# Kernel optimization log

Measured on AMD Instinct MI355X. Metric: run time of the kernel, lower is better.

The kernel has to match this reference:

```python
import jax, jax.numpy as jnp
import numpy as np

BN_EPS = 1e-5


def setup_inputs() -> dict:
    key = jax.random.key(0)
    ks = jax.random.split(key, 16)
    N, E, IN, H, A, L = 50000, 400000, 128, 192, 192, 3
    s = 0.02
    inp = {
        "x": jax.random.normal(ks[0], (N, IN), dtype=jnp.float32),
        "edge_index": jax.random.randint(ks[1], (2, E), 0, N, dtype=jnp.int32),
        "seed_idx": 123,
        "proj_w": jax.random.normal(ks[2], (IN, H), dtype=jnp.float32) * s,
        "proj_b": jnp.zeros((H,), dtype=jnp.float32),
        "mlp1_w": jax.random.normal(ks[3], (L, H, H), dtype=jnp.float32) * s,
        "mlp1_b": jnp.zeros((L, H), dtype=jnp.float32),
        "mlp2_w": jax.random.normal(ks[4], (L, H, H), dtype=jnp.float32) * s,
        "mlp2_b": jnp.zeros((L, H), dtype=jnp.float32),
        "eps": jnp.zeros((L,), dtype=jnp.float32),  # GIN train_eps init 0
        "bn_g": jnp.ones((L, H), dtype=jnp.float32),
        "bn_b": jnp.zeros((L, H), dtype=jnp.float32),
        "W1": jax.random.normal(ks[5], (H, A), dtype=jnp.float32) * s,
        "W2": jax.random.normal(ks[6], (H, A), dtype=jnp.float32) * s,
        "w_attn": jax.random.normal(ks[7], (A,), dtype=jnp.float32) * s,
        "cls_w": jax.random.normal(ks[8], (H,), dtype=jnp.float32) * s,
        "cls_b": jnp.zeros((1,), dtype=jnp.float32),
    }
    return inp


def _forward(x, edge_index, seed_idx, proj_w, proj_b, mlp1_w, mlp1_b,
             mlp2_w, mlp2_b, eps, bn_g, bn_b, W1, W2, w_attn, cls_w, cls_b):
    N = x.shape[0]
    src, dst = edge_index[0], edge_index[1]
    h = jax.nn.relu(x @ proj_w + proj_b)  # [N, H]
    L = mlp1_w.shape[0]
    for l in range(L):
        # GINConv: mlp((1+eps)*h + sum_{j->i} h_j) via scatter-add on dst
        agg = jax.ops.segment_sum(h[src], dst, num_segments=N)  # [N, H]
        z = (1.0 + eps[l]) * h + agg
        z = jax.nn.relu(z @ mlp1_w[l] + mlp1_b[l]) @ mlp2_w[l] + mlp2_b[l]
        # BatchNorm over nodes (batch statistics)
        mu = z.mean(axis=0)
        var = z.var(axis=0)
        z = (z - mu) * jax.lax.rsqrt(var + BN_EPS) * bn_g[l] + bn_b[l]
        h = jax.nn.relu(z)  # dropout is identity in eval
    h_seed = h[seed_idx]  # valid seed index branch
    zat = jnp.tanh(h @ W1 + h_seed @ W2)          # [N, A]
    e = jax.nn.leaky_relu(zat @ w_attn, 0.2)      # [N]
    alpha = jax.nn.softmax(e, axis=0)             # [N]
    readout = alpha @ h                           # [H]
    logit = readout @ cls_w + cls_b               # [1]
    return logit, alpha


def reference(x, edge_index, seed_idx, proj_w, proj_b, mlp1_w, mlp1_b,
              mlp2_w, mlp2_b, eps, bn_g, bn_b, W1, W2, w_attn, cls_w, cls_b):
    return _forward(x, edge_index, seed_idx, proj_w, proj_b, mlp1_w, mlp1_b,
                    mlp2_w, mlp2_b, eps, bn_g, bn_b, W1, W2, w_attn, cls_w, cls_b)
```

## Files before the change

kernel.cpp:

```cpp
#include <hip/hip_runtime.h>
#include <hip/hip_bf16.h>

#define N_NODES 50000
#define N_EDGES 400000
#define DIM_IN  128
#define DIM_H   192
#define N_LAYERS 3
#define BN_EPSF 1e-5f
#define SCAN_NBLK 49
#define INV_N (1.f / N_NODES)
#define NSHADOW 8
#define SSTRIDE 384
#define WTP_BLOCKS 138

typedef __attribute__((ext_vector_type(8))) short short8;
typedef __attribute__((ext_vector_type(4))) float floatx4;

union FragU { uint4 u; short8 s; };

__device__ __forceinline__ float relu_f(float x) { return x > 0.f ? x : 0.f; }
__device__ __forceinline__ unsigned short f2bf(float x) {
  __hip_bfloat16 h = __float2bfloat16(x);
  return *reinterpret_cast<unsigned short*>(&h);
}
__device__ __forceinline__ float bf2f(unsigned short b) {
  return __uint_as_float(((unsigned)b) << 16);
}
__device__ __forceinline__ float bflo(unsigned u) { return __uint_as_float(u << 16); }
__device__ __forceinline__ float bfhi(unsigned u) { return __uint_as_float(u & 0xffff0000u); }

__device__ __forceinline__ unsigned char f2f8(float v) {
  return (unsigned char)(__builtin_amdgcn_cvt_pk_fp8_f32(v, v, 0, false) & 0xff);
}
template <int SEL>
__device__ __forceinline__ float f8dec(unsigned u) {
  return __builtin_amdgcn_cvt_f32_fp8((int)u, SEL);
}

__global__ void k_wtp_hist(const float* __restrict__ m1, const float* __restrict__ m2,
                           const float* __restrict__ wa, const float* __restrict__ pw,
                           uint4* __restrict__ outp,
                           const int* __restrict__ edge, int* __restrict__ cnt) {
  if (blockIdx.x < WTP_BLOCKS) {
    const int NH = 7 * 24 * 192;
    const int NP = 16 * 192;
    int idx = blockIdx.x * 256 + threadIdx.x;
    if (idx >= NH + NP) return;
    union { uint4 u; unsigned short h[8]; } fr;
    if (idx < NH) {
      int mat = idx / (24 * 192);
      int rem = idx - mat * (24 * 192);
      int kidx = rem / 192, col = rem - kidx * 192;
      const float* src = mat < 3 ? m1 + (size_t)mat * (DIM_H * DIM_H)
                       : (mat < 6 ? m2 + (size_t)(mat - 3) * (DIM_H * DIM_H) : wa);
#pragma unroll
      for (int t = 0; t < 8; ++t) fr.h[t] = f2bf(src[(size_t)(kidx * 8 + t) * DIM_H + col]);
    } else {
      int rem = idx - NH;
      int kidx = rem / 192, col = rem - kidx * 192;
#pragma unroll
      for (int t = 0; t < 8; ++t) fr.h[t] = f2bf(pw[(size_t)(kidx * 8 + t) * DIM_H + col]);
    }
    outp[idx] = fr.u;
  } else {
    int e = (blockIdx.x - WTP_BLOCKS) * 256 + threadIdx.x;
    if (e < N_EDGES) atomicAdd(&cnt[edge[N_EDGES + e]], 1);
  }
}

__global__ void k_scanA(const int* __restrict__ deg, int* __restrict__ part, int* __restrict__ bsum) {
  __shared__ int buf[1024];
  int g = blockIdx.x * 1024 + threadIdx.x;
  int v = (g < N_NODES) ? deg[g] : 0;
  buf[threadIdx.x] = v;
  __syncthreads();
  for (int off = 1; off < 1024; off <<= 1) {
    int t = (threadIdx.x >= off) ? buf[threadIdx.x - off] : 0;
    __syncthreads();
    buf[threadIdx.x] += t;
    __syncthreads();
  }
  if (g < N_NODES) part[g] = buf[threadIdx.x];
  if (threadIdx.x == 1023) bsum[blockIdx.x] = buf[1023];
}

__global__ void k_scanC(const int* __restrict__ part, const int* __restrict__ bsum,
                        int* __restrict__ rowptr, int* __restrict__ cursor) {
  __shared__ int excl[64];
  int tid = threadIdx.x;
  if (tid < 64) {
    int own = (tid < SCAN_NBLK) ? bsum[tid] : 0;
    int v = own;
    for (int off = 1; off < 64; off <<= 1) {
      int t = __shfl_up(v, off);
      if (tid >= off) v += t;
    }
    excl[tid] = v - own;
  }
  __syncthreads();
  int g = blockIdx.x * 256 + tid;
  if (g == 0) { rowptr[0] = 0; cursor[0] = 0; }
  if (g < N_NODES) {
    int v = part[g] + excl[g >> 10];
    rowptr[g + 1] = v;
    if (g + 1 < N_NODES) cursor[g + 1] = v;
  }
}

__global__ void k_fill(const int* __restrict__ edge, int* __restrict__ cursor, int* __restrict__ csr) {
  int e = blockIdx.x * 256 + threadIdx.x;
  if (e < N_EDGES) {
    int s = edge[e];
    int d = edge[N_EDGES + e];
    int pos = atomicAdd(&cursor[d], 1);
    csr[pos] = s;
  }
}

template <bool BN>
__global__ void k_agg(const unsigned char* __restrict__ z, const int* __restrict__ rowptr,
                      const int* __restrict__ csr, const float* __restrict__ stats,
                      const float* __restrict__ bng, const float* __restrict__ bnb,
                      const float* __restrict__ eps, int l, unsigned short* __restrict__ outA) {
  int wid = threadIdx.x >> 6, lane = threadIdx.x & 63;
  int node = blockIdx.x * 4 + wid;
  if (node >= N_NODES || lane >= 48) return;
  int c = lane * 4;
  float4 sc4 = {1.f, 1.f, 1.f, 1.f}, sh4 = {0.f, 0.f, 0.f, 0.f};
  if (BN) {
    float4 st = {0.f, 0.f, 0.f, 0.f}, sq = {0.f, 0.f, 0.f, 0.f};
#pragma unroll
    for (int g = 0; g < NSHADOW; ++g) {
      const float* sp = stats + g * SSTRIDE;
      float4 a = *(const float4*)(sp + c);
      float4 b = *(const float4*)(sp + DIM_H + c);
      st.x += a.x; st.y += a.y; st.z += a.z; st.w += a.w;
      sq.x += b.x; sq.y += b.y; sq.z += b.z; sq.w += b.w;
    }
    float4 g4 = *(const float4*)(bng + c);
    float4 b4 = *(const float4*)(bnb + c);
    float mu, rs;
    mu = st.x * INV_N; rs = rsqrtf(sq.x * INV_N - mu * mu + BN_EPSF); sc4.x = g4.x * rs; sh4.x = b4.x - mu * sc4.x;
    mu = st.y * INV_N; rs = rsqrtf(sq.y * INV_N - mu * mu + BN_EPSF); sc4.y = g4.y * rs; sh4.y = b4.y - mu * sc4.y;
    mu = st.z * INV_N; rs = rsqrtf(sq.z * INV_N - mu * mu + BN_EPSF); sc4.z = g4.z * rs; sh4.z = b4.z - mu * sc4.z;
    mu = st.w * INV_N; rs = rsqrtf(sq.w * INV_N - mu * mu + BN_EPSF); sc4.w = g4.w * rs; sh4.w = b4.w - mu * sc4.w;
  }
  float a0 = 0.f, a1 = 0.f, a2 = 0.f, a3 = 0.f;
  int beg = rowptr[node], end = rowptr[node + 1];
  unsigned us = *(const unsigned*)(z + (size_t)node * DIM_H + c);
#define ACCU(U)                                                          \
  {                                                                      \
    float v0 = f8dec<0>(U), v1 = f8dec<1>(U);                            \
    float v2 = f8dec<2>(U), v3 = f8dec<3>(U);                            \
    if (BN) {                                                            \
      v0 = relu_f(fmaf(v0, sc4.x, sh4.x));                               \
      v1 = relu_f(fmaf(v1, sc4.y, sh4.y));                               \
      v2 = relu_f(fmaf(v2, sc4.z, sh4.z));                               \
      v3 = relu_f(fmaf(v3, sc4.w, sh4.w));                               \
    }                                                                    \
    a0 += v0; a1 += v1; a2 += v2; a3 += v3;                              \
  }
  int j = beg;
  for (; j + 4 <= end; j += 4) {
    int s0 = csr[j], s1 = csr[j + 1], s2 = csr[j + 2], s3 = csr[j + 3];
    unsigned u0 = *(const unsigned*)(z + (size_t)s0 * DIM_H + c);
    unsigned u1 = *(const unsigned*)(z + (size_t)s1 * DIM_H + c);
    unsigned u2 = *(const unsigned*)(z + (size_t)s2 * DIM_H + c);
    unsigned u3 = *(const unsigned*)(z + (size_t)s3 * DIM_H + c);
    ACCU(u0) ACCU(u1) ACCU(u2) ACCU(u3)
  }
  for (; j < end; ++j) {
    int s0 = csr[j];
    unsigned u0 = *(const unsigned*)(z + (size_t)s0 * DIM_H + c);
    ACCU(u0)
  }
#undef ACCU
  float ep = 1.f + eps[l];
  {
    float v0 = f8dec<0>(us), v1 = f8dec<1>(us), v2 = f8dec<2>(us), v3 = f8dec<3>(us);
    if (BN) {
      v0 = relu_f(fmaf(v0, sc4.x, sh4.x));
      v1 = relu_f(fmaf(v1, sc4.y, sh4.y));
      v2 = relu_f(fmaf(v2, sc4.z, sh4.z));
      v3 = relu_f(fmaf(v3, sc4.w, sh4.w));
    }
    a0 += ep * v0; a1 += ep * v1; a2 += ep * v2; a3 += ep * v3;
  }
  uint2 o;
  o.x = (unsigned)f2bf(a0) | ((unsigned)f2bf(a1) << 16);
  o.y = (unsigned)f2bf(a2) | ((unsigned)f2bf(a3) << 16);
  *(uint2*)(outA + (size_t)node * DIM_H + c) = o;
}

template <int KS>
__device__ __forceinline__ void load_b(const uint4* __restrict__ Bp, int colbase, int kq, int lr,
                                       FragU (&b)[KS][3]) {
#pragma unroll
  for (int ks = 0; ks < KS; ++ks)
#pragma unroll
    for (int n = 0; n < 3; ++n)
      b[ks][n].u = Bp[(ks * 4 + kq) * 192 + colbase + n * 16 + lr];
}

template <int KS, int MT>
__device__ __forceinline__ void mfma_stage_pre(const uint4* a_lds, const FragU (&b)[KS][3],
                                               int kq, int lr, floatx4 (&acc)[MT][3]) {
#pragma unroll
  for (int ks = 0; ks < KS; ++ks) {
    int kidx = ks * 4 + kq;
    FragU a[MT];
#pragma unroll
    for (int m = 0; m < MT; ++m) a[m].u = a_lds[kidx * (MT * 16) + m * 16 + lr];
#pragma unroll
    for (int n = 0; n < 3; ++n)
#pragma unroll
      for (int m = 0; m < MT; ++m)
        acc[m][n] = __builtin_amdgcn_mfma_f32_16x16x32_bf16(a[m].s, b[ks][n].s, acc[m][n], 0, 0, 0);
  }
}

__global__ __launch_bounds__(256) void k_proj(const float* __restrict__ A,
                                              const uint4* __restrict__ Bp,
                                              const float* __restrict__ bias,
                                              unsigned char* __restrict__ C) {
  __shared__ uint4 a_lds[16 * 64];
  const int tid = threadIdx.x;
  const int rbase = blockIdx.x * 64;
  const int lane = tid & 63, w = tid >> 6;
  const int kq = lane >> 4, lr = lane & 15;
  const int colbase = w * 48;
  FragU b[4][3];
  load_b<4>(Bp, colbase, kq, lr, b);
#pragma unroll
  for (int i = 0; i < 4; ++i) {
    int row = tid >> 2, kidx = i * 4 + (tid & 3);
    int gr = rbase + row;
    gr = gr < N_NODES ? gr : N_NODES - 1;
    const float* ap = A + (size_t)gr * DIM_IN + kidx * 8;
    float4 v0 = *(const float4*)ap;
    float4 v1 = *(const float4*)(ap + 4);
    union { uint4 u; unsigned short h[8]; } fr;
    fr.h[0] = f2bf(v0.x); fr.h[1] = f2bf(v0.y); fr.h[2] = f2bf(v0.z); fr.h[3] = f2bf(v0.w);
    fr.h[4] = f2bf(v1.x); fr.h[5] = f2bf(v1.y); fr.h[6] = f2bf(v1.z); fr.h[7] = f2bf(v1.w);
    a_lds[kidx * 64 + row] = fr.u;
  }
  __syncthreads();
  floatx4 acc[4][3];
  floatx4 zero4 = {0.f, 0.f, 0.f, 0.f};
#pragma unroll
  for (int m = 0; m < 4; ++m)
#pragma unroll
    for (int n = 0; n < 3; ++n) acc[m][n] = zero4;
  mfma_stage_pre<4, 4>(a_lds, b, kq, lr, acc);
#pragma unroll
  for (int n = 0; n < 3; ++n) {
    int col = colbase + n * 16 + lr;
    float bb = bias[col];
#pragma unroll
    for (int m = 0; m < 4; ++m)
#pragma unroll
      for (int j = 0; j < 4; ++j) {
        int row = rbase + m * 16 + kq * 4 + j;
        if (row < N_NODES) C[(size_t)row * DIM_H + col] = f2f8(relu_f(acc[m][n][j] + bb));
      }
  }
}

__device__ __forceinline__ void z_epi(floatx4 (&acc)[2][3], unsigned short* zl, const float* __restrict__ b1,
                                      int colbase, int kq, int lr) {
#pragma unroll
  for (int n = 0; n < 3; ++n) {
    int col = colbase + n * 16 + lr;
    float bb = b1[col];
#pragma unroll
    for (int m = 0; m < 2; ++m)
#pragma unroll
      for (int j = 0; j < 4; ++j) {
        int rowl = m * 16 + kq * 4 + j;
        zl[(col >> 3) * 256 + rowl * 8 + (col & 7)] = f2bf(relu_f(acc[m][n][j] + bb));
      }
  }
}

template <bool F8>
__device__ __forceinline__ void out_epi(floatx4 (&acc)[2][3], void* __restrict__ Zout,
                                        const float* __restrict__ b2, int rb, int colbase, int kq, int lr,
                                        float (&s3)[3], float (&q3)[3]) {
#pragma unroll
  for (int n = 0; n < 3; ++n) {
    int col = colbase + n * 16 + lr;
    float bb = b2[col];
#pragma unroll
    for (int m = 0; m < 2; ++m)
#pragma unroll
      for (int j = 0; j < 4; ++j) {
        int row = rb + m * 16 + kq * 4 + j;
        if (row < N_NODES) {
          float v = acc[m][n][j] + bb;
          if (F8)
            ((unsigned char*)Zout)[(size_t)row * DIM_H + col] = f2f8(v);
          else
            ((unsigned short*)Zout)[(size_t)row * DIM_H + col] = f2bf(v);
          s3[n] += v;
          q3[n] += v * v;
        }
      }
  }
}

template <bool F8>
__global__ __launch_bounds__(256, 3) void k_mlp(const unsigned short* __restrict__ A,
                                                const uint4* __restrict__ B1p, const float* __restrict__ b1,
                                                const uint4* __restrict__ B2p, const float* __restrict__ b2,
                                                void* __restrict__ Zout, float* __restrict__ stats) {
  __shared__ uint4 a_lds[2][24 * 32];
  const int tid = threadIdx.x;
  const int rbase = blockIdx.x * 64;
  const int lane = tid & 63, w = tid >> 6;
  const int kq = lane >> 4, lr = lane & 15;
  const int colbase = w * 48;
  uint4 areg[2][3];
  const int arow = tid >> 3;
#pragma unroll
  for (int t = 0; t < 2; ++t) {
    int agr = rbase + t * 32 + arow;
    agr = agr < N_NODES ? agr : N_NODES - 1;
#pragma unroll
    for (int i = 0; i < 3; ++i) {
      int kidx = i * 8 + (tid & 7);
      areg[t][i] = *(const uint4*)(A + (size_t)agr * DIM_H + kidx * 8);
    }
  }
  FragU b1r[6][3];
  load_b<6>(B1p, colbase, kq, lr, b1r);
#pragma unroll
  for (int t = 0; t < 2; ++t)
#pragma unroll
    for (int i = 0; i < 3; ++i) {
      int kidx = i * 8 + (tid & 7);
      a_lds[t][kidx * 32 + arow] = areg[t][i];
    }
  __syncthreads();
  floatx4 zero4 = {0.f, 0.f, 0.f, 0.f};
  floatx4 acc0[2][3], acc1[2][3];
#pragma unroll
  for (int m = 0; m < 2; ++m)
#pragma unroll
    for (int n = 0; n < 3; ++n) { acc0[m][n] = zero4; acc1[m][n] = zero4; }
  mfma_stage_pre<6, 2>(a_lds[0], b1r, kq, lr, acc0);
  mfma_stage_pre<6, 2>(a_lds[1], b1r, kq, lr, acc1);
  FragU b2r[6][3];
  load_b<6>(B2p, colbase, kq, lr, b2r);
  __syncthreads();
  z_epi(acc0, (unsigned short*)a_lds[0], b1, colbase, kq, lr);
  z_epi(acc1, (unsigned short*)a_lds[1], b1, colbase, kq, lr);
  __syncthreads();
#pragma unroll
  for (int m = 0; m < 2; ++m)
#pragma unroll
    for (int n = 0; n < 3; ++n) { acc0[m][n] = zero4; acc1[m][n] = zero4; }
  mfma_stage_pre<6, 2>(a_lds[0], b2r, kq, lr, acc0);
  mfma_stage_pre<6, 2>(a_lds[1], b2r, kq, lr, acc1);
  float s3[3] = {0.f, 0.f, 0.f}, q3[3] = {0.f, 0.f, 0.f};
  out_epi<F8>(acc0, Zout, b2, rbase, colbase, kq, lr, s3, q3);
  out_epi<F8>(acc1, Zout, b2, rbase + 32, colbase, kq, lr, s3, q3);
  __syncthreads();
  float* ps = (float*)a_lds;
  float* pq = ps + DIM_H * 4;
#pragma unroll
  for (int n = 0; n < 3; ++n) {
    int col = colbase + n * 16 + lr;
    ps[col * 4 + kq] = s3[n];
    pq[col * 4 + kq] = q3[n];
  }
  __syncthreads();
  if (tid < DIM_H) {
    float ts = 0.f, tq = 0.f;
#pragma unroll
    for (int g = 0; g < 4; ++g) {
      ts += ps[tid * 4 + g];
      tq += pq[tid * 4 + g];
    }
    float* sp = stats + (blockIdx.x & (NSHADOW - 1)) * SSTRIDE;
    atomicAdd(&sp[tid], ts);
    atomicAdd(&sp[DIM_H + tid], tq);
  }
}

__global__ __launch_bounds__(256, 3) void k_attnm(const unsigned short* __restrict__ Zin,
                                                  const float* __restrict__ stats,
                                                  const float* __restrict__ bng,
                                                  const float* __restrict__ bnb,
                                                  const uint4* __restrict__ Bp,
                                                  const int* __restrict__ seedp,
                                                  const float* __restrict__ W2,
                                                  const float* __restrict__ wat,
                                                  float* __restrict__ p, float* __restrict__ scal,
                                                  float* __restrict__ rdoutS) {
  __shared__ uint4 a_lds[24 * 64];
  __shared__ float part[64][65];
  __shared__ float cs[DIM_H], ch[DIM_H], hs[DIM_H], s2l[DIM_H];
  __shared__ float pe_lds[64];
  const int tid = threadIdx.x;
  const int rbase = blockIdx.x * 64;
  const int lane = tid & 63, w = tid >> 6;
  const int kq = lane >> 4, lr = lane & 15;
  const int colbase = w * 48;
  FragU b[6][3];
  load_b<6>(Bp, colbase, kq, lr, b);
  if (tid < DIM_H) {
    float ts = 0.f, tq = 0.f;
#pragma unroll
    for (int g = 0; g < NSHADOW; ++g) {
      ts += stats[g * SSTRIDE + tid];
      tq += stats[g * SSTRIDE + DIM_H + tid];
    }
    float mu = ts * INV_N;
    float rs = rsqrtf(tq * INV_N - mu * mu + BN_EPSF);
    float sc = bng[tid] * rs;
    float sh = bnb[tid] - mu * sc;
    cs[tid] = sc;
    ch[tid] = sh;
    int seed = seedp[0];
    hs[tid] = relu_f(bf2f(Zin[(size_t)seed * DIM_H + tid]) * sc + sh);
  }
  __syncthreads();
#pragma unroll
  for (int i = 0; i < 6; ++i) {
    int row = tid >> 2, kidx = i * 4 + (tid & 3);
    int gr = rbase + row;
    gr = gr < N_NODES ? gr : N_NODES - 1;
    union { uint4 u; unsigned short h[8]; } v, o;
    v.u = *(const uint4*)(Zin + (size_t)gr * DIM_H + kidx * 8);
#pragma unroll
    for (int t = 0; t < 8; ++t)
      o.h[t] = f2bf(relu_f(bf2f(v.h[t]) * cs[kidx * 8 + t] + ch[kidx * 8 + t]));
    a_lds[kidx * 64 + row] = o.u;
  }
  if (tid < DIM_H) {
    float t0 = 0.f, t1 = 0.f, t2 = 0.f, t3 = 0.f;
    for (int k = 0; k < DIM_H; k += 4) {
      t0 = fmaf(hs[k + 0], W2[(size_t)(k + 0) * DIM_H + tid], t0);
      t1 = fmaf(hs[k + 1], W2[(size_t)(k + 1) * DIM_H + tid], t1);
      t2 = fmaf(hs[k + 2], W2[(size_t)(k + 2) * DIM_H + tid], t2);
      t3 = fmaf(hs[k + 3], W2[(size_t)(k + 3) * DIM_H + tid], t3);
    }
    s2l[tid] = (t0 + t1) + (t2 + t3);
  }
  __syncthreads();
  floatx4 zero4 = {0.f, 0.f, 0.f, 0.f};
  floatx4 acc[4][3];
#pragma unroll
  for (int m = 0; m < 4; ++m)
#pragma unroll
    for (int n = 0; n < 3; ++n) acc[m][n] = zero4;
  mfma_stage_pre<6, 4>(a_lds, b, kq, lr, acc);
  float pv[16];
#pragma unroll
  for (int t = 0; t < 16; ++t) pv[t] = 0.f;
#pragma unroll
  for (int n = 0; n < 3; ++n) {
    int col = colbase + n * 16 + lr;
    float s2c = s2l[col];
    float wv = wat[col];
#pragma unroll
    for (int m = 0; m < 4; ++m)
#pragma unroll
      for (int j = 0; j < 4; ++j) {
        float xv = acc[m][n][j] + s2c;
        xv = fminf(fmaxf(xv, -10.f), 10.f);
        float t = __expf(2.f * xv);
        pv[m * 4 + j] = fmaf((t - 1.f) / (t + 1.f), wv, pv[m * 4 + j]);
      }
  }
#pragma unroll
  for (int m = 0; m < 4; ++m)
#pragma unroll
    for (int j = 0; j < 4; ++j)
      part[m * 16 + kq * 4 + j][w * 16 + lr] = pv[m * 4 + j];
  __syncthreads();
  if (tid < 64) {
    float s = 0.f;
#pragma unroll
    for (int i = 0; i < 64; ++i) s += part[tid][i];
    s = s > 0.f ? s : 0.2f * s;
    float pe = __expf(s);
    int gr = rbase + tid;
    bool valid = gr < N_NODES;
    if (valid) p[gr] = pe;
    pe = valid ? pe : 0.f;
    pe_lds[tid] = pe;
    float red = pe;
#pragma unroll
    for (int off = 32; off > 0; off >>= 1) red += __shfl_xor(red, off);
    if (tid == 0) atomicAdd(&scal[0], red);
  }
  __syncthreads();
  if (tid < DIM_H) {
    const unsigned short* al = (const unsigned short*)a_lds;
    int base = (tid >> 3) * 512 + (tid & 7);
    float s = 0.f;
    for (int it = 0; it < 64; ++it) {
      int row = (it + tid) & 63;
      s = fmaf(pe_lds[row], bf2f(al[base + row * 8]), s);
    }
    atomicAdd(&rdoutS[(blockIdx.x & (NSHADOW - 1)) * DIM_H + tid], s);
  }
}

__global__ void k_alpha(const float* __restrict__ p, const float* __restrict__ scal,
                        float* __restrict__ alpha) {
  int i = blockIdx.x * 256 + threadIdx.x;
  if (i < N_NODES) alpha[i] = p[i] * (1.f / scal[0]);
}

__global__ void k_logit(const float* __restrict__ rdoutS, const float* __restrict__ scal,
                        const float* __restrict__ cw, const float* __restrict__ cb,
                        float* __restrict__ out) {
  __shared__ float buf[256];
  int tid = threadIdx.x;
  float v = 0.f;
  if (tid < DIM_H) {
    float s = 0.f;
#pragma unroll
    for (int g = 0; g < NSHADOW; ++g) s += rdoutS[g * DIM_H + tid];
    v = s * cw[tid];
  }
  buf[tid] = v;
  __syncthreads();
  for (int s = 128; s > 0; s >>= 1) {
    if (tid < s) buf[tid] += buf[tid + s];
    __syncthreads();
  }
  if (tid == 0) out[0] = buf[0] * (1.f / scal[0]) + cb[0];
}

extern "C" void kernel_launch(void* const* d_in, const int* in_sizes, int n_in,
                              void* d_out, int out_size, void* d_ws, size_t ws_size,
                              hipStream_t stream) {
  const float* x      = (const float*)d_in[0];
  const int*   edge   = (const int*)d_in[1];
  const int*   seedp  = (const int*)d_in[2];
  const float* proj_w = (const float*)d_in[3];
  const float* proj_b = (const float*)d_in[4];
  const float* mlp1_w = (const float*)d_in[5];
  const float* mlp1_b = (const float*)d_in[6];
  const float* mlp2_w = (const float*)d_in[7];
  const float* mlp2_b = (const float*)d_in[8];
  const float* eps    = (const float*)d_in[9];
  const float* bn_g   = (const float*)d_in[10];
  const float* bn_b   = (const float*)d_in[11];
  const float* W1     = (const float*)d_in[12];
  const float* W2     = (const float*)d_in[13];
  const float* w_attn = (const float*)d_in[14];
  const float* cls_w  = (const float*)d_in[15];
  const float* cls_b  = (const float*)d_in[16];
  float* out = (float*)d_out;

  char* ws = (char*)d_ws;
  size_t off = 0;
  auto alloc = [&](size_t bytes) -> void* {
    void* p = ws + off;
    off = (off + bytes + 255) & ~(size_t)255;
    return p;
  };
  unsigned char*  f8a    = (unsigned char*)alloc((size_t)N_NODES * DIM_H);
  unsigned char*  f8b    = (unsigned char*)alloc((size_t)N_NODES * DIM_H);
  unsigned short* aggOut = (unsigned short*)alloc((size_t)N_NODES * DIM_H * 2);
  unsigned short* zbf    = (unsigned short*)alloc((size_t)N_NODES * DIM_H * 2);
  float* pbuf   = (float*)alloc((size_t)N_NODES * 4);
  int* rowptr   = (int*)alloc((size_t)(N_NODES + 1) * 4);
  int* csr      = (int*)alloc((size_t)N_EDGES * 4);
  int* part     = (int*)alloc((size_t)N_NODES * 4);
  int* bsum     = (int*)alloc(64 * 4);
  size_t zbeg = off;
  int* cursor   = (int*)alloc((size_t)(N_NODES + 1) * 4);
  float* statsA = (float*)alloc((size_t)N_LAYERS * NSHADOW * SSTRIDE * 4);
  float* scalrd = (float*)alloc((size_t)(64 + NSHADOW * DIM_H) * 4);
  size_t zend = off;
  float* scal   = scalrd;
  float* rdoutS = scalrd + 64;
  uint4* WTall  = (uint4*)alloc((size_t)(7 * 24 * 192 + 16 * 192) * 16);

  float* statsL[N_LAYERS];
  for (int l = 0; l < N_LAYERS; ++l) statsL[l] = statsA + (size_t)l * NSHADOW * SSTRIDE;

  const uint4* B1p[N_LAYERS] = {WTall, WTall + 4608, WTall + 2 * 4608};
  const uint4* B2p[N_LAYERS] = {WTall + 3 * 4608, WTall + 4 * 4608, WTall + 5 * 4608};
  const uint4* Bap = WTall + 6 * 4608;
  const uint4* Bpp = WTall + 7 * 4608;

  const int GRID64 = (N_NODES + 63) / 64;
  const int AGG_GRID = (N_NODES + 3) / 4;

  hipMemsetAsync(ws + zbeg, 0, zend - zbeg, stream);

  k_wtp_hist<<<WTP_BLOCKS + (N_EDGES + 255) / 256, 256, 0, stream>>>(
      mlp1_w, mlp2_w, W1, proj_w, WTall, edge, cursor);

  k_scanA<<<SCAN_NBLK, 1024, 0, stream>>>(cursor, part, bsum);
  k_scanC<<<(N_NODES + 255) / 256, 256, 0, stream>>>(part, bsum, rowptr, cursor);
  k_fill<<<(N_EDGES + 255) / 256, 256, 0, stream>>>(edge, cursor, csr);

  k_proj<<<GRID64, 256, 0, stream>>>(x, Bpp, proj_b, f8a);

  k_agg<false><<<AGG_GRID, 256, 0, stream>>>(f8a, rowptr, csr, statsL[0], bn_g, bn_b, eps, 0, aggOut);
  k_mlp<true><<<GRID64, 256, 0, stream>>>(aggOut, B1p[0], mlp1_b, B2p[0], mlp2_b, f8b, statsL[0]);
  k_agg<true><<<AGG_GRID, 256, 0, stream>>>(f8b, rowptr, csr, statsL[0], bn_g, bn_b, eps, 1, aggOut);
  k_mlp<true><<<GRID64, 256, 0, stream>>>(aggOut, B1p[1], mlp1_b + DIM_H, B2p[1], mlp2_b + DIM_H, f8a, statsL[1]);
  k_agg<true><<<AGG_GRID, 256, 0, stream>>>(f8a, rowptr, csr, statsL[1], bn_g + DIM_H, bn_b + DIM_H, eps, 2, aggOut);
  k_mlp<false><<<GRID64, 256, 0, stream>>>(aggOut, B1p[2], mlp1_b + 2 * DIM_H, B2p[2], mlp2_b + 2 * DIM_H, zbf, statsL[2]);

  const float* g2 = bn_g + (size_t)2 * DIM_H;
  const float* b2c = bn_b + (size_t)2 * DIM_H;

  k_attnm<<<GRID64, 256, 0, stream>>>(zbf, statsL[2], g2, b2c, Bap, seedp, W2, w_attn, pbuf, scal, rdoutS);
  k_alpha<<<(N_NODES + 255) / 256, 256, 0, stream>>>(pbuf, scal, out + 1);
  k_logit<<<1, 256, 0, stream>>>(rdoutS, scal, cls_w, cls_b, out);
}
```

Before: 288.8 us.

## Fuse neighbor aggregation into MLP kernel, writing aggregated rows to LDS

Merges the gather/segment-sum kernel into the per-layer MLP kernel. Each 64-row block now aggregates its own nodes, with each wave handling 16 rows in sequence, and writes the bf16 results straight into the LDS A-tile. This removes the intermediate aggOut buffer (its global write and read-back) and three kernel launches. In exchange, the gather runs on fewer concurrent waves per node, which may reduce memory-level parallelism for the latency-bound random loads, and launch bounds are raised to 4 blocks per CU.

```diff
diff --git a/kernel.cpp b/kernel.cpp
--- a/kernel.cpp
+++ b/kernel.cpp
@@ -117,81 +117,6 @@
   }
 }
 
-template <bool BN>
-__global__ void k_agg(const unsigned char* __restrict__ z, const int* __restrict__ rowptr,
-                      const int* __restrict__ csr, const float* __restrict__ stats,
-                      const float* __restrict__ bng, const float* __restrict__ bnb,
-                      const float* __restrict__ eps, int l, unsigned short* __restrict__ outA) {
-  int wid = threadIdx.x >> 6, lane = threadIdx.x & 63;
-  int node = blockIdx.x * 4 + wid;
-  if (node >= N_NODES || lane >= 48) return;
-  int c = lane * 4;
-  float4 sc4 = {1.f, 1.f, 1.f, 1.f}, sh4 = {0.f, 0.f, 0.f, 0.f};
-  if (BN) {
-    float4 st = {0.f, 0.f, 0.f, 0.f}, sq = {0.f, 0.f, 0.f, 0.f};
-#pragma unroll
-    for (int g = 0; g < NSHADOW; ++g) {
-      const float* sp = stats + g * SSTRIDE;
-      float4 a = *(const float4*)(sp + c);
-      float4 b = *(const float4*)(sp + DIM_H + c);
-      st.x += a.x; st.y += a.y; st.z += a.z; st.w += a.w;
-      sq.x += b.x; sq.y += b.y; sq.z += b.z; sq.w += b.w;
-    }
-    float4 g4 = *(const float4*)(bng + c);
-    float4 b4 = *(const float4*)(bnb + c);
-    float mu, rs;
-    mu = st.x * INV_N; rs = rsqrtf(sq.x * INV_N - mu * mu + BN_EPSF); sc4.x = g4.x * rs; sh4.x = b4.x - mu * sc4.x;
-    mu = st.y * INV_N; rs = rsqrtf(sq.y * INV_N - mu * mu + BN_EPSF); sc4.y = g4.y * rs; sh4.y = b4.y - mu * sc4.y;
-    mu = st.z * INV_N; rs = rsqrtf(sq.z * INV_N - mu * mu + BN_EPSF); sc4.z = g4.z * rs; sh4.z = b4.z - mu * sc4.z;
-    mu = st.w * INV_N; rs = rsqrtf(sq.w * INV_N - mu * mu + BN_EPSF); sc4.w = g4.w * rs; sh4.w = b4.w - mu * sc4.w;
-  }
-  float a0 = 0.f, a1 = 0.f, a2 = 0.f, a3 = 0.f;
-  int beg = rowptr[node], end = rowptr[node + 1];
-  unsigned us = *(const unsigned*)(z + (size_t)node * DIM_H + c);
-#define ACCU(U)                                                          \
-  {                                                                      \
-    float v0 = f8dec<0>(U), v1 = f8dec<1>(U);                            \
-    float v2 = f8dec<2>(U), v3 = f8dec<3>(U);                            \
-    if (BN) {                                                            \
-      v0 = relu_f(fmaf(v0, sc4.x, sh4.x));                               \
-      v1 = relu_f(fmaf(v1, sc4.y, sh4.y));                               \
-      v2 = relu_f(fmaf(v2, sc4.z, sh4.z));                               \
-      v3 = relu_f(fmaf(v3, sc4.w, sh4.w));                               \
-    }                                                                    \
-    a0 += v0; a1 += v1; a2 += v2; a3 += v3;                              \
-  }
-  int j = beg;
-  for (; j + 4 <= end; j += 4) {
-    int s0 = csr[j], s1 = csr[j + 1], s2 = csr[j + 2], s3 = csr[j + 3];
-    unsigned u0 = *(const unsigned*)(z + (size_t)s0 * DIM_H + c);
-    unsigned u1 = *(const unsigned*)(z + (size_t)s1 * DIM_H + c);
-    unsigned u2 = *(const unsigned*)(z + (size_t)s2 * DIM_H + c);
-    unsigned u3 = *(const unsigned*)(z + (size_t)s3 * DIM_H + c);
-    ACCU(u0) ACCU(u1) ACCU(u2) ACCU(u3)
-  }
-  for (; j < end; ++j) {
-    int s0 = csr[j];
-    unsigned u0 = *(const unsigned*)(z + (size_t)s0 * DIM_H + c);
-    ACCU(u0)
-  }
-#undef ACCU
-  float ep = 1.f + eps[l];
-  {
-    float v0 = f8dec<0>(us), v1 = f8dec<1>(us), v2 = f8dec<2>(us), v3 = f8dec<3>(us);
-    if (BN) {
-      v0 = relu_f(fmaf(v0, sc4.x, sh4.x));
-      v1 = relu_f(fmaf(v1, sc4.y, sh4.y));
-      v2 = relu_f(fmaf(v2, sc4.z, sh4.z));
-      v3 = relu_f(fmaf(v3, sc4.w, sh4.w));
-    }
-    a0 += ep * v0; a1 += ep * v1; a2 += ep * v2; a3 += ep * v3;
-  }
-  uint2 o;
-  o.x = (unsigned)f2bf(a0) | ((unsigned)f2bf(a1) << 16);
-  o.y = (unsigned)f2bf(a2) | ((unsigned)f2bf(a3) << 16);
-  *(uint2*)(outA + (size_t)node * DIM_H + c) = o;
-}
-
 template <int KS>
 __device__ __forceinline__ void load_b(const uint4* __restrict__ Bp, int colbase, int kq, int lr,
                                        FragU (&b)[KS][3]) {
@@ -308,38 +233,98 @@
   }
 }
 
-template <bool F8>
-__global__ __launch_bounds__(256, 3) void k_mlp(const unsigned short* __restrict__ A,
-                                                const uint4* __restrict__ B1p, const float* __restrict__ b1,
-                                                const uint4* __restrict__ B2p, const float* __restrict__ b2,
-                                                void* __restrict__ Zout, float* __restrict__ stats) {
+template <bool BN, bool F8OUT>
+__global__ __launch_bounds__(256, 4) void k_aggmlp(
+    const unsigned char* __restrict__ z, const int* __restrict__ rowptr,
+    const int* __restrict__ csr, const float* __restrict__ statsPrev,
+    const float* __restrict__ bng, const float* __restrict__ bnb,
+    const float* __restrict__ eps, int l,
+    const uint4* __restrict__ B1p, const float* __restrict__ b1,
+    const uint4* __restrict__ B2p, const float* __restrict__ b2,
+    void* __restrict__ Zout, float* __restrict__ statsOut) {
   __shared__ uint4 a_lds[2][24 * 32];
   const int tid = threadIdx.x;
   const int rbase = blockIdx.x * 64;
   const int lane = tid & 63, w = tid >> 6;
   const int kq = lane >> 4, lr = lane & 15;
   const int colbase = w * 48;
-  uint4 areg[2][3];
-  const int arow = tid >> 3;
-#pragma unroll
-  for (int t = 0; t < 2; ++t) {
-    int agr = rbase + t * 32 + arow;
-    agr = agr < N_NODES ? agr : N_NODES - 1;
-#pragma unroll
-    for (int i = 0; i < 3; ++i) {
-      int kidx = i * 8 + (tid & 7);
-      areg[t][i] = *(const uint4*)(A + (size_t)agr * DIM_H + kidx * 8);
+  float4 sc4 = {1.f, 1.f, 1.f, 1.f}, sh4 = {0.f, 0.f, 0.f, 0.f};
+  const int c = lane * 4;
+  if (BN && lane < 48) {
+    float4 st = {0.f, 0.f, 0.f, 0.f}, sq = {0.f, 0.f, 0.f, 0.f};
+#pragma unroll
+    for (int g = 0; g < NSHADOW; ++g) {
+      const float* sp = statsPrev + g * SSTRIDE;
+      float4 a = *(const float4*)(sp + c);
+      float4 b = *(const float4*)(sp + DIM_H + c);
+      st.x += a.x; st.y += a.y; st.z += a.z; st.w += a.w;
+      sq.x += b.x; sq.y += b.y; sq.z += b.z; sq.w += b.w;
+    }
+    float4 g4 = *(const float4*)(bng + c);
+    float4 b4 = *(const float4*)(bnb + c);
+    float mu, rs;
+    mu = st.x * INV_N; rs = rsqrtf(sq.x * INV_N - mu * mu + BN_EPSF); sc4.x = g4.x * rs; sh4.x = b4.x - mu * sc4.x;
+    mu = st.y * INV_N; rs = rsqrtf(sq.y * INV_N - mu * mu + BN_EPSF); sc4.y = g4.y * rs; sh4.y = b4.y - mu * sc4.y;
+    mu = st.z * INV_N; rs = rsqrtf(sq.z * INV_N - mu * mu + BN_EPSF); sc4.z = g4.z * rs; sh4.z = b4.z - mu * sc4.z;
+    mu = st.w * INV_N; rs = rsqrtf(sq.w * INV_N - mu * mu + BN_EPSF); sc4.w = g4.w * rs; sh4.w = b4.w - mu * sc4.w;
+  }
+  const float ep = 1.f + eps[l];
+  for (int rr = 0; rr < 16; ++rr) {
+    int r = w * 16 + rr;
+    int node = rbase + r;
+    node = node < N_NODES ? node : N_NODES - 1;
+    if (lane < 48) {
+      int beg = rowptr[node], end = rowptr[node + 1];
+      unsigned us = *(const unsigned*)(z + (size_t)node * DIM_H + c);
+      float a0 = 0.f, a1 = 0.f, a2 = 0.f, a3 = 0.f;
+#define ACCU(U)                                                          \
+      {                                                                  \
+        float v0 = f8dec<0>(U), v1 = f8dec<1>(U);                        \
+        float v2 = f8dec<2>(U), v3 = f8dec<3>(U);                        \
+        if (BN) {                                                        \
+          v0 = relu_f(fmaf(v0, sc4.x, sh4.x));                           \
+          v1 = relu_f(fmaf(v1, sc4.y, sh4.y));                           \
+          v2 = relu_f(fmaf(v2, sc4.z, sh4.z));                           \
+          v3 = relu_f(fmaf(v3, sc4.w, sh4.w));                           \
+        }                                                                \
+        a0 += v0; a1 += v1; a2 += v2; a3 += v3;                          \
+      }
+      int j = beg;
+      for (; j + 4 <= end; j += 4) {
+        int s0 = csr[j], s1 = csr[j + 1], s2 = csr[j + 2], s3 = csr[j + 3];
+        unsigned u0 = *(const unsigned*)(z + (size_t)s0 * DIM_H + c);
+        unsigned u1 = *(const unsigned*)(z + (size_t)s1 * DIM_H + c);
+        unsigned u2 = *(const unsigned*)(z + (size_t)s2 * DIM_H + c);
+        unsigned u3 = *(const unsigned*)(z + (size_t)s3 * DIM_H + c);
+        ACCU(u0) ACCU(u1) ACCU(u2) ACCU(u3)
+      }
+      for (; j < end; ++j) {
+        int s0 = csr[j];
+        unsigned u0 = *(const unsigned*)(z + (size_t)s0 * DIM_H + c);
+        ACCU(u0)
+      }
+#undef ACCU
+      {
+        float v0 = f8dec<0>(us), v1 = f8dec<1>(us), v2 = f8dec<2>(us), v3 = f8dec<3>(us);
+        if (BN) {
+          v0 = relu_f(fmaf(v0, sc4.x, sh4.x));
+          v1 = relu_f(fmaf(v1, sc4.y, sh4.y));
+          v2 = relu_f(fmaf(v2, sc4.z, sh4.z));
+          v3 = relu_f(fmaf(v3, sc4.w, sh4.w));
+        }
+        a0 += ep * v0; a1 += ep * v1; a2 += ep * v2; a3 += ep * v3;
+      }
+      int t = r >> 5, rowl = r & 31;
+      unsigned short* zl = (unsigned short*)(a_lds[t]);
+      int pos = ((c >> 3) * 32 + rowl) * 8 + (c & 7);
+      uint2 o;
+      o.x = (unsigned)f2bf(a0) | ((unsigned)f2bf(a1) << 16);
+      o.y = (unsigned)f2bf(a2) | ((unsigned)f2bf(a3) << 16);
+      *(uint2*)(zl + pos) = o;
     }
   }
   FragU b1r[6][3];
   load_b<6>(B1p, colbase, kq, lr, b1r);
-#pragma unroll
-  for (int t = 0; t < 2; ++t)
-#pragma unroll
-    for (int i = 0; i < 3; ++i) {
-      int kidx = i * 8 + (tid & 7);
-      a_lds[t][kidx * 32 + arow] = areg[t][i];
-    }
   __syncthreads();
   floatx4 zero4 = {0.f, 0.f, 0.f, 0.f};
   floatx4 acc0[2][3], acc1[2][3];
@@ -362,8 +347,8 @@
   mfma_stage_pre<6, 2>(a_lds[0], b2r, kq, lr, acc0);
   mfma_stage_pre<6, 2>(a_lds[1], b2r, kq, lr, acc1);
   float s3[3] = {0.f, 0.f, 0.f}, q3[3] = {0.f, 0.f, 0.f};
-  out_epi<F8>(acc0, Zout, b2, rbase, colbase, kq, lr, s3, q3);
-  out_epi<F8>(acc1, Zout, b2, rbase + 32, colbase, kq, lr, s3, q3);
+  out_epi<F8OUT>(acc0, Zout, b2, rbase, colbase, kq, lr, s3, q3);
+  out_epi<F8OUT>(acc1, Zout, b2, rbase + 32, colbase, kq, lr, s3, q3);
   __syncthreads();
   float* ps = (float*)a_lds;
   float* pq = ps + DIM_H * 4;
@@ -381,7 +366,7 @@
       ts += ps[tid * 4 + g];
       tq += pq[tid * 4 + g];
     }
-    float* sp = stats + (blockIdx.x & (NSHADOW - 1)) * SSTRIDE;
+    float* sp = statsOut + (blockIdx.x & (NSHADOW - 1)) * SSTRIDE;
     atomicAdd(&sp[tid], ts);
     atomicAdd(&sp[DIM_H + tid], tq);
   }
@@ -564,10 +549,9 @@
     off = (off + bytes + 255) & ~(size_t)255;
     return p;
   };
-  unsigned char*  f8a    = (unsigned char*)alloc((size_t)N_NODES * DIM_H);
-  unsigned char*  f8b    = (unsigned char*)alloc((size_t)N_NODES * DIM_H);
-  unsigned short* aggOut = (unsigned short*)alloc((size_t)N_NODES * DIM_H * 2);
-  unsigned short* zbf    = (unsigned short*)alloc((size_t)N_NODES * DIM_H * 2);
+  unsigned char*  f8a = (unsigned char*)alloc((size_t)N_NODES * DIM_H);
+  unsigned char*  f8b = (unsigned char*)alloc((size_t)N_NODES * DIM_H);
+  unsigned short* zbf = (unsigned short*)alloc((size_t)N_NODES * DIM_H * 2);
   float* pbuf   = (float*)alloc((size_t)N_NODES * 4);
   int* rowptr   = (int*)alloc((size_t)(N_NODES + 1) * 4);
   int* csr      = (int*)alloc((size_t)N_EDGES * 4);
@@ -591,7 +575,6 @@
   const uint4* Bpp = WTall + 7 * 4608;
 
   const int GRID64 = (N_NODES + 63) / 64;
-  const int AGG_GRID = (N_NODES + 3) / 4;
 
   hipMemsetAsync(ws + zbeg, 0, zend - zbeg, stream);
 
@@ -604,12 +587,15 @@
 
   k_proj<<<GRID64, 256, 0, stream>>>(x, Bpp, proj_b, f8a);
 
-  k_agg<false><<<AGG_GRID, 256, 0, stream>>>(f8a, rowptr, csr, statsL[0], bn_g, bn_b, eps, 0, aggOut);
-  k_mlp<true><<<GRID64, 256, 0, stream>>>(aggOut, B1p[0], mlp1_b, B2p[0], mlp2_b, f8b, statsL[0]);
-  k_agg<true><<<AGG_GRID, 256, 0, stream>>>(f8b, rowptr, csr, statsL[0], bn_g, bn_b, eps, 1, aggOut);
-  k_mlp<true><<<GRID64, 256, 0, stream>>>(aggOut, B1p[1], mlp1_b + DIM_H, B2p[1], mlp2_b + DIM_H, f8a, statsL[1]);
-  k_agg<true><<<AGG_GRID, 256, 0, stream>>>(f8a, rowptr, csr, statsL[1], bn_g + DIM_H, bn_b + DIM_H, eps, 2, aggOut);
-  k_mlp<false><<<GRID64, 256, 0, stream>>>(aggOut, B1p[2], mlp1_b + 2 * DIM_H, B2p[2], mlp2_b + 2 * DIM_H, zbf, statsL[2]);
+  k_aggmlp<false, true><<<GRID64, 256, 0, stream>>>(
+      f8a, rowptr, csr, statsL[0], bn_g, bn_b, eps, 0,
+      B1p[0], mlp1_b, B2p[0], mlp2_b, f8b, statsL[0]);
+  k_aggmlp<true, true><<<GRID64, 256, 0, stream>>>(
+      f8b, rowptr, csr, statsL[0], bn_g, bn_b, eps, 1,
+      B1p[1], mlp1_b + DIM_H, B2p[1], mlp2_b + DIM_H, f8a, statsL[1]);
+  k_aggmlp<true, false><<<GRID64, 256, 0, stream>>>(
+      f8a, rowptr, csr, statsL[1], bn_g + DIM_H, bn_b + DIM_H, eps, 2,
+      B1p[2], mlp1_b + 2 * DIM_H, B2p[2], mlp2_b + 2 * DIM_H, zbf, statsL[2]);
 
   const float* g2 = bn_g + (size_t)2 * DIM_H;
   const float* b2c = bn_b + (size_t)2 * DIM_H;
```

After: 292.9 us. About the same (+1.4%).
